# Optimization experiments

Measured on AMD Instinct MI355X. Metric: run time of the kernel, lower is better.

## Reference

```python
import jax, jax.numpy as jnp
import numpy as np

B, S, D, H = 4, 2048, 1024, 16
DH = D // H
MAX_SEQ = 2048
OUT = 1024


def setup_inputs() -> dict:
    key = jax.random.key(0)
    ks = jax.random.split(key, 10)
    inp = {
        "x": jax.random.normal(ks[0], (B, S, D), dtype=jnp.float32),
        "src_key_padding_mask": jnp.ones((B, S), dtype=jnp.float32),  # 1 = valid token
        "pos_emb": jax.random.normal(ks[1], (1, MAX_SEQ, D), dtype=jnp.float32),
        "ln_gamma": jnp.ones((D,), dtype=jnp.float32),
        "ln_beta": jnp.zeros((D,), dtype=jnp.float32),
        "in_proj_weight": jax.random.normal(ks[2], (3 * D, D), dtype=jnp.float32) * (1.0 / np.sqrt(D)),
        "in_proj_bias": jnp.zeros((3 * D,), dtype=jnp.float32),
        "out_proj_weight": jax.random.normal(ks[3], (D, D), dtype=jnp.float32) * (1.0 / np.sqrt(D)),
        "out_proj_bias": jnp.zeros((D,), dtype=jnp.float32),
        "to_out_weight": jax.random.normal(ks[4], (OUT, D), dtype=jnp.float32) * (1.0 / np.sqrt(D)),
        "to_out_bias": jnp.zeros((OUT,), dtype=jnp.float32),
    }
    return inp


def _layernorm(x, gamma, beta, eps=1e-5):
    mu = jnp.mean(x, axis=-1, keepdims=True)
    var = jnp.mean(jnp.square(x - mu), axis=-1, keepdims=True)
    return (x - mu) * jax.lax.rsqrt(var + eps) * gamma + beta


def reference(x, src_key_padding_mask, pos_emb, ln_gamma, ln_beta,
              in_proj_weight, in_proj_bias, out_proj_weight, out_proj_bias,
              to_out_weight, to_out_bias):
    seq = x.shape[1]
    xn = _layernorm(x, ln_gamma, ln_beta)
    xp = xn + pos_emb[:, :seq, :]  # [B,S,D]

    # PyTorch quirk: 1.0 - mask.long() is a FLOAT tensor -> treated as ADDITIVE mask.
    add_mask = (1.0 - src_key_padding_mask)[:, None, None, :]  # [B,1,1,S]

    qkv = xp @ in_proj_weight.T + in_proj_bias  # [B,S,3D]
    q, k, v = jnp.split(qkv, 3, axis=-1)
    # [B,H,S,DH]
    q = q.reshape(B, seq, H, DH).transpose(0, 2, 1, 3)
    k = k.reshape(B, seq, H, DH).transpose(0, 2, 1, 3)
    v = v.reshape(B, seq, H, DH).transpose(0, 2, 1, 3)

    scores = jnp.einsum("bhqd,bhkd->bhqk", q, k) / jnp.sqrt(jnp.float32(DH))
    scores = scores + add_mask
    attn = jax.nn.softmax(scores, axis=-1)
    o = jnp.einsum("bhqk,bhkd->bhqd", attn, v)  # [B,H,S,DH]
    o = o.transpose(0, 2, 1, 3).reshape(B, seq, D)
    attn_out = o @ out_proj_weight.T + out_proj_bias

    return (xp + attn_out) @ to_out_weight.T + to_out_bias
```

## Files before the change

### kernel.cpp

```cpp
#include <hip/hip_runtime.h>
#include <stdint.h>
#include <stddef.h>

typedef unsigned short u16;
typedef __bf16 bf16x8 __attribute__((ext_vector_type(8)));
typedef float floatx4 __attribute__((ext_vector_type(4)));

#define B_  4
#define S_  2048
#define D_  1024
#define H_  16
#define DH_ 64

__device__ __forceinline__ float b2f(u16 u) {
  union { unsigned u; float f; } c; c.u = ((unsigned)u) << 16; return c.f;
}
__device__ __forceinline__ u16 f2b(float f) {
  union { float f; unsigned u; } c; c.f = f;
  unsigned u = c.u;
  u += 0x7fffu + ((u >> 16) & 1u);
  return (u16)(u >> 16);
}

__device__ __forceinline__ void gld_lds16(const u16* g, u16* l) {
  __builtin_amdgcn_global_load_lds(
      (const __attribute__((address_space(1))) unsigned int*)g,
      (__attribute__((address_space(3))) unsigned int*)l, 16, 0, 0);
}

__global__ __launch_bounds__(256) void cvt_f32_bf16(
    const float* __restrict__ src, u16* __restrict__ dst, int n)
{
  int i = (blockIdx.x * 256 + threadIdx.x) * 4;
  if (i >= n) return;
  float4 v = *(const float4*)(src + i);
  u16 o[4] __attribute__((aligned(8)));
  o[0] = f2b(v.x); o[1] = f2b(v.y); o[2] = f2b(v.z); o[3] = f2b(v.w);
  *(uint2*)(dst + i) = *(uint2*)o;
}

__global__ __launch_bounds__(256) void ln_pos_kernel(
    const float* __restrict__ x, const float* __restrict__ pos,
    const float* __restrict__ gamma, const float* __restrict__ beta,
    u16* __restrict__ xp)
{
  const int row = blockIdx.x;
  const int s = row & (S_ - 1);
  const int t = threadIdx.x;
  const int lane = t & 63, w = t >> 6;

  float4 xv = *(const float4*)(x + (size_t)row * D_ + t * 4);
  float f[4] = {xv.x, xv.y, xv.z, xv.w};
  float sum = f[0] + f[1] + f[2] + f[3];
  float sq  = f[0]*f[0] + f[1]*f[1] + f[2]*f[2] + f[3]*f[3];
#pragma unroll
  for (int m = 1; m < 64; m <<= 1) {
    sum += __shfl_xor(sum, m);
    sq  += __shfl_xor(sq, m);
  }
  __shared__ float red[8];
  if (lane == 0) { red[w] = sum; red[4 + w] = sq; }
  __syncthreads();
  sum = red[0] + red[1] + red[2] + red[3];
  sq  = red[4] + red[5] + red[6] + red[7];
  const float mu = sum * (1.f / D_);
  const float rstd = rsqrtf(fmaxf(sq * (1.f / D_) - mu * mu, 0.f) + 1e-5f);

  float4 gv = *(const float4*)(gamma + t * 4);
  float4 bv = *(const float4*)(beta + t * 4);
  float4 pv = *(const float4*)(pos + (size_t)s * D_ + t * 4);
  float g[4] = {gv.x, gv.y, gv.z, gv.w};
  float bb[4] = {bv.x, bv.y, bv.z, bv.w};
  float pp[4] = {pv.x, pv.y, pv.z, pv.w};
  u16 ov[4] __attribute__((aligned(8)));
#pragma unroll
  for (int i = 0; i < 4; ++i)
    ov[i] = f2b((f[i] - mu) * rstd * g[i] + bb[i] + pp[i]);
  *(uint2*)(xp + (size_t)row * D_ + t * 4) = *(uint2*)ov;
}

template<int HAS_BIAS, int HAS_RES, int OUT_F32>
__global__ __launch_bounds__(256) void gemm_bt(
    const u16* A, const u16* __restrict__ Bm,
    const float* __restrict__ bias, const u16* res,
    void* Cv, int M, int N, int K, int lda, int ldc)
{
  __shared__ u16 As[128 * 32];
  __shared__ u16 Bs[128 * 32];
  const int tid = threadIdx.x;
  const int lane = tid & 63, w = tid >> 6;
  const int quad = lane >> 4, l4 = lane & 15;
  const int wm = (w >> 1) * 64, wn = (w & 1) * 64;
  const int m0 = blockIdx.y * 128, n0 = blockIdx.x * 128;

  const u16* Ag = A + (size_t)m0 * lda;
  const u16* Bg = Bm + (size_t)n0 * K;

  const int s0 = tid, s1 = tid + 256;
  const int r0 = s0 >> 2, c0 = ((s0 & 3) - (r0 >> 1)) & 3;
  const int r1 = s1 >> 2, c1 = ((s1 & 3) - (r1 >> 1)) & 3;
  const int pA = (quad + (l4 >> 1)) & 3;

  floatx4 acc[4][4] = {};

  for (int k0 = 0; k0 < K; k0 += 32) {
    __syncthreads();
    gld_lds16(Ag + (size_t)r0 * lda + k0 + c0 * 8, &As[s0 * 8]);
    gld_lds16(Ag + (size_t)r1 * lda + k0 + c1 * 8, &As[s1 * 8]);
    gld_lds16(Bg + (size_t)r0 * K + k0 + c0 * 8, &Bs[s0 * 8]);
    gld_lds16(Bg + (size_t)r1 * K + k0 + c1 * 8, &Bs[s1 * 8]);
    __syncthreads();
    bf16x8 af[4], bfr[4];
#pragma unroll
    for (int i = 0; i < 4; ++i)
      af[i] = *(const bf16x8*)&As[(wm + i * 16 + l4) * 32 + pA * 8];
#pragma unroll
    for (int j = 0; j < 4; ++j)
      bfr[j] = *(const bf16x8*)&Bs[(wn + j * 16 + l4) * 32 + pA * 8];
#pragma unroll
    for (int i = 0; i < 4; ++i)
#pragma unroll
      for (int j = 0; j < 4; ++j)
        acc[i][j] = __builtin_amdgcn_mfma_f32_16x16x32_bf16(af[i], bfr[j], acc[i][j], 0, 0, 0);
  }

#pragma unroll
  for (int i = 0; i < 4; ++i) {
#pragma unroll
    for (int j = 0; j < 4; ++j) {
      const int col = n0 + wn + j * 16 + l4;
      float bvv = 0.f;
      if (HAS_BIAS) bvv = bias[col];
#pragma unroll
      for (int r = 0; r < 4; ++r) {
        const int row = m0 + wm + i * 16 + quad * 4 + r;
        float v = acc[i][j][r] + bvv;
        if (HAS_RES) v += b2f(res[(size_t)row * ldc + col]);
        v = fminf(fmaxf(v, -60000.f), 60000.f);
        if (OUT_F32) ((float*)Cv)[(size_t)row * ldc + col] = v;
        else         ((u16*)Cv)[(size_t)row * ldc + col] = f2b(v);
      }
    }
  }
}

__global__ __launch_bounds__(256) void attn_kernel(
    u16* qkv, const float* __restrict__ mask)
{
  __shared__ u16 Qs[64 * 64];
  __shared__ u16 Ks[128 * 64];
  __shared__ u16 Vt[64 * 136];
  __shared__ u16 Ps[64 * 136];

  const int tid = threadIdx.x;
  const int lane = tid & 63, w = tid >> 6;
  const int quad = lane >> 4, l4 = lane & 15;
  const int qb = blockIdx.x;
  const int bh = blockIdx.y;
  const int b = bh >> 4, h = bh & 15;
  const int q0 = qb * 64;

  const size_t rstr = 3 * D_;
  u16* qbase = qkv + (size_t)b * S_ * rstr + h * DH_;

  {
    int sA = tid, sB = tid + 256;
    int ra = sA >> 3, ca = ((sA & 7) - ra) & 7;
    int rb = sB >> 3, cb = ((sB & 7) - rb) & 7;
    gld_lds16(qbase + (size_t)(q0 + ra) * rstr + ca * 8, &Qs[sA * 8]);
    gld_lds16(qbase + (size_t)(q0 + rb) * rstr + cb * 8, &Qs[sB * 8]);
  }

  floatx4 acc_o[4] = {};
  float l_run[4] = {0.f, 0.f, 0.f, 0.f};

  for (int j = 0; j < 16; ++j) {
    __syncthreads();
    const u16* kbase = qkv + ((size_t)b * S_ + j * 128) * rstr + D_ + h * DH_;
#pragma unroll
    for (int t = 0; t < 4; ++t) {
      int sidx = tid + t * 256;
      int r = sidx >> 3, ch = ((sidx & 7) - r) & 7;
      gld_lds16(kbase + (size_t)r * rstr + ch * 8, &Ks[sidx * 8]);
    }
    {
      const u16* vbase = qkv + ((size_t)b * S_ + j * 128) * rstr + 2 * D_ + h * DH_;
      int s = tid & 127, d0 = (tid >> 7) * 32;
      const u16* vp = vbase + (size_t)s * rstr + d0;
      u16 v[32] __attribute__((aligned(16)));
      *(uint4*)(v)      = *(const uint4*)(vp);
      *(uint4*)(v + 8)  = *(const uint4*)(vp + 8);
      *(uint4*)(v + 16) = *(const uint4*)(vp + 16);
      *(uint4*)(v + 24) = *(const uint4*)(vp + 24);
#pragma unroll
      for (int d = 0; d < 32; ++d) Vt[(d0 + d) * 136 + s] = v[d];
    }
    __syncthreads();

    floatx4 accs[8] = {};
#pragma unroll
    for (int kc = 0; kc < 2; ++kc) {
      const int rq = w * 16 + l4;
      bf16x8 af = *(const bf16x8*)&Qs[rq * 64 + (((kc * 4 + quad) + rq) & 7) * 8];
#pragma unroll
      for (int tj = 0; tj < 8; ++tj) {
        const int rk = tj * 16 + l4;
        bf16x8 bfr = *(const bf16x8*)&Ks[rk * 64 + (((kc * 4 + quad) + rk) & 7) * 8];
        accs[tj] = __builtin_amdgcn_mfma_f32_16x16x32_bf16(af, bfr, accs[tj], 0, 0, 0);
      }
    }

    const float* mrow = mask + (size_t)b * S_ + j * 128;
    float rsum[4] = {0.f, 0.f, 0.f, 0.f};
#pragma unroll
    for (int tj = 0; tj < 8; ++tj) {
      const float addm = 1.0f - mrow[tj * 16 + l4];
#pragma unroll
      for (int r = 0; r < 4; ++r) {
        float sc = fminf(accs[tj][r] * 0.125f + addm, 30.f);
        float p = __expf(sc);
        rsum[r] += p;
        Ps[(w * 16 + quad * 4 + r) * 136 + tj * 16 + l4] = f2b(p);
      }
    }
#pragma unroll
    for (int r = 0; r < 4; ++r) {
      float v = rsum[r];
      v += __shfl_xor(v, 1);
      v += __shfl_xor(v, 2);
      v += __shfl_xor(v, 4);
      v += __shfl_xor(v, 8);
      l_run[r] += v;
    }

    asm volatile("s_waitcnt lgkmcnt(0)" ::: "memory");

#pragma unroll
    for (int kc = 0; kc < 4; ++kc) {
      bf16x8 af = *(const bf16x8*)&Ps[(w * 16 + l4) * 136 + kc * 32 + quad * 8];
#pragma unroll
      for (int tn = 0; tn < 4; ++tn) {
        bf16x8 bfr = *(const bf16x8*)&Vt[(tn * 16 + l4) * 136 + kc * 32 + quad * 8];
        acc_o[tn] = __builtin_amdgcn_mfma_f32_16x16x32_bf16(af, bfr, acc_o[tn], 0, 0, 0);
      }
    }
  }

#pragma unroll
  for (int tn = 0; tn < 4; ++tn) {
#pragma unroll
    for (int r = 0; r < 4; ++r) {
      const int row = q0 + w * 16 + quad * 4 + r;
      const int col = h * DH_ + tn * 16 + l4;
      qkv[((size_t)b * S_ + row) * rstr + col] = f2b(acc_o[tn][r] / l_run[r]);
    }
  }
}

extern "C" void kernel_launch(void* const* d_in, const int* in_sizes, int n_in,
                              void* d_out, int out_size, void* d_ws, size_t ws_size,
                              hipStream_t stream) {
  const float* x    = (const float*)d_in[0];
  const float* mask = (const float*)d_in[1];
  const float* pos  = (const float*)d_in[2];
  const float* gam  = (const float*)d_in[3];
  const float* bet  = (const float*)d_in[4];
  const float* wqkv = (const float*)d_in[5];
  const float* bqkv = (const float*)d_in[6];
  const float* wo   = (const float*)d_in[7];
  const float* bo   = (const float*)d_in[8];
  const float* wt   = (const float*)d_in[9];
  const float* bt   = (const float*)d_in[10];
  float* out = (float*)d_out;

  char* ws = (char*)d_ws;
  u16* qkvb = (u16*)(ws);
  u16* xp   = (u16*)(ws + (size_t)50331648);

  u16* wqkv_b = (u16*)d_out;
  u16* wo_b   = (u16*)((char*)d_out + (size_t)6291456);
  u16* wt_b   = qkvb;

  const int nqkv = 3 * D_ * D_;
  const int nd   = D_ * D_;

  cvt_f32_bf16<<<nqkv / 1024, 256, 0, stream>>>(wqkv, wqkv_b, nqkv);
  cvt_f32_bf16<<<nd   / 1024, 256, 0, stream>>>(wo,   wo_b,   nd);
  ln_pos_kernel<<<B_ * S_, 256, 0, stream>>>(x, pos, gam, bet, xp);
  gemm_bt<1, 0, 0><<<dim3(3 * D_ / 128, B_ * S_ / 128), 256, 0, stream>>>(
      xp, wqkv_b, bqkv, nullptr, qkvb, B_ * S_, 3 * D_, D_, D_, 3 * D_);
  attn_kernel<<<dim3(S_ / 64, B_ * H_), 256, 0, stream>>>(qkvb, mask);
  gemm_bt<1, 1, 0><<<dim3(D_ / 128, B_ * S_ / 128), 256, 0, stream>>>(
      qkvb, wo_b, bo, xp, xp, B_ * S_, D_, D_, 3 * D_, D_);
  cvt_f32_bf16<<<nd / 1024, 256, 0, stream>>>(wt, wt_b, nd);
  gemm_bt<1, 0, 1><<<dim3(D_ / 128, B_ * S_ / 128), 256, 0, stream>>>(
      xp, wt_b, bt, nullptr, out, B_ * S_, D_, D_, D_, D_);
}
```

Measured before the change: 478.2 us.

## Keep Q and P fragments in registers in attention, drop Qs/Ps shared buffers

The attention kernel computes S^T (K as the A operand, Q held in registers), so each lane owns a query column. It turns probabilities into bf16 pairs with v_cvt_pk_bf16_f32 and rearranges them through permlane swaps into the A-operand layout of the PV MFMA, removing the Ps round trip through LDS and the Qs staging buffer. This cuts LDS traffic and footprint, allowing 4 blocks per CU via launch bounds, and adds setprio around the MFMAs. The cost is more register pressure and a reliance on exact lane-permutation semantics.

```diff
diff --git a/kernel.cpp b/kernel.cpp
--- a/kernel.cpp
+++ b/kernel.cpp
@@ -27,6 +27,17 @@
       (const __attribute__((address_space(1))) unsigned int*)g,
       (__attribute__((address_space(3))) unsigned int*)l, 16, 0, 0);
 }
+
+__device__ __forceinline__ unsigned cvtpk(float lo, float hi) {
+  unsigned r;
+  asm("v_cvt_pk_bf16_f32 %0, %1, %2" : "=v"(r) : "v"(lo), "v"(hi));
+  return r;
+}
+
+#define PL32(a, b) asm("v_permlane32_swap_b32 %0, %1" : "+v"(a), "+v"(b))
+#define PL16(a, b) asm("v_permlane16_swap_b32 %0, %1" : "+v"(a), "+v"(b))
+
+union B8 { unsigned u[4]; bf16x8 v; };
 
 __global__ __launch_bounds__(256) void cvt_f32_bf16(
     const float* __restrict__ src, u16* __restrict__ dst, int n)
@@ -144,13 +155,11 @@
   }
 }
 
-__global__ __launch_bounds__(256) void attn_kernel(
+__global__ __launch_bounds__(256, 4) void attn_kernel(
     u16* qkv, const float* __restrict__ mask)
 {
-  __shared__ u16 Qs[64 * 64];
   __shared__ u16 Ks[128 * 64];
   __shared__ u16 Vt[64 * 136];
-  __shared__ u16 Ps[64 * 136];
 
   const int tid = threadIdx.x;
   const int lane = tid & 63, w = tid >> 6;
@@ -163,16 +172,15 @@
   const size_t rstr = 3 * D_;
   u16* qbase = qkv + (size_t)b * S_ * rstr + h * DH_;
 
+  bf16x8 qfrag[2];
   {
-    int sA = tid, sB = tid + 256;
-    int ra = sA >> 3, ca = ((sA & 7) - ra) & 7;
-    int rb = sB >> 3, cb = ((sB & 7) - rb) & 7;
-    gld_lds16(qbase + (size_t)(q0 + ra) * rstr + ca * 8, &Qs[sA * 8]);
-    gld_lds16(qbase + (size_t)(q0 + rb) * rstr + cb * 8, &Qs[sB * 8]);
+    const u16* qp = qbase + (size_t)(q0 + w * 16 + l4) * rstr + quad * 8;
+    qfrag[0] = *(const bf16x8*)(qp);
+    qfrag[1] = *(const bf16x8*)(qp + 32);
   }
 
   floatx4 acc_o[4] = {};
-  float l_run[4] = {0.f, 0.f, 0.f, 0.f};
+  float l_run = 0.f;
 
   for (int j = 0; j < 16; ++j) {
     __syncthreads();
@@ -180,8 +188,8 @@
 #pragma unroll
     for (int t = 0; t < 4; ++t) {
       int sidx = tid + t * 256;
-      int r = sidx >> 3, ch = ((sidx & 7) - r) & 7;
-      gld_lds16(kbase + (size_t)r * rstr + ch * 8, &Ks[sidx * 8]);
+      int rr = sidx >> 3, ch = ((sidx & 7) - rr) & 7;
+      gld_lds16(kbase + (size_t)rr * rstr + ch * 8, &Ks[sidx * 8]);
     }
     {
       const u16* vbase = qkv + ((size_t)b * S_ + j * 128) * rstr + 2 * D_ + h * DH_;
@@ -199,60 +207,59 @@
 
     floatx4 accs[8] = {};
 #pragma unroll
-    for (int kc = 0; kc < 2; ++kc) {
-      const int rq = w * 16 + l4;
-      bf16x8 af = *(const bf16x8*)&Qs[rq * 64 + (((kc * 4 + quad) + rq) & 7) * 8];
+    for (int kc = 0; kc < 2; ++kc)
 #pragma unroll
       for (int tj = 0; tj < 8; ++tj) {
         const int rk = tj * 16 + l4;
-        bf16x8 bfr = *(const bf16x8*)&Ks[rk * 64 + (((kc * 4 + quad) + rk) & 7) * 8];
-        accs[tj] = __builtin_amdgcn_mfma_f32_16x16x32_bf16(af, bfr, accs[tj], 0, 0, 0);
+        bf16x8 kf = *(const bf16x8*)&Ks[rk * 64 + (((kc * 4 + quad) + rk) & 7) * 8];
+        accs[tj] = __builtin_amdgcn_mfma_f32_16x16x32_bf16(kf, qfrag[kc], accs[tj], 0, 0, 0);
       }
-    }
-
-    const float* mrow = mask + (size_t)b * S_ + j * 128;
-    float rsum[4] = {0.f, 0.f, 0.f, 0.f};
+
+    const float* mrow = mask + (size_t)b * S_ + j * 128 + quad * 4;
+    float rsum = 0.f;
+    unsigned pk[8][2];
 #pragma unroll
     for (int tj = 0; tj < 8; ++tj) {
-      const float addm = 1.0f - mrow[tj * 16 + l4];
-#pragma unroll
-      for (int r = 0; r < 4; ++r) {
-        float sc = fminf(accs[tj][r] * 0.125f + addm, 30.f);
-        float p = __expf(sc);
-        rsum[r] += p;
-        Ps[(w * 16 + quad * 4 + r) * 136 + tj * 16 + l4] = f2b(p);
-      }
-    }
-#pragma unroll
-    for (int r = 0; r < 4; ++r) {
-      float v = rsum[r];
-      v += __shfl_xor(v, 1);
-      v += __shfl_xor(v, 2);
-      v += __shfl_xor(v, 4);
-      v += __shfl_xor(v, 8);
-      l_run[r] += v;
-    }
-
-    asm volatile("s_waitcnt lgkmcnt(0)" ::: "memory");
+      float4 mv = *(const float4*)(mrow + tj * 16);
+      float p0 = __expf(fminf(fmaf(accs[tj][0], 0.125f, 1.0f - mv.x), 30.f));
+      float p1 = __expf(fminf(fmaf(accs[tj][1], 0.125f, 1.0f - mv.y), 30.f));
+      float p2 = __expf(fminf(fmaf(accs[tj][2], 0.125f, 1.0f - mv.z), 30.f));
+      float p3 = __expf(fminf(fmaf(accs[tj][3], 0.125f, 1.0f - mv.w), 30.f));
+      rsum += (p0 + p1) + (p2 + p3);
+      pk[tj][0] = cvtpk(p0, p1);
+      pk[tj][1] = cvtpk(p2, p3);
+    }
+    rsum += __shfl_xor(rsum, 16);
+    rsum += __shfl_xor(rsum, 32);
+    l_run += rsum;
 
 #pragma unroll
     for (int kc = 0; kc < 4; ++kc) {
-      bf16x8 af = *(const bf16x8*)&Ps[(w * 16 + l4) * 136 + kc * 32 + quad * 8];
+      unsigned x0 = pk[2 * kc][0], x1 = pk[2 * kc + 1][0];
+      unsigned y0 = pk[2 * kc][1], y1 = pk[2 * kc + 1][1];
+      PL32(x0, x1); PL32(y0, y1);
+      PL16(x0, x1); PL16(y0, y1);
+      B8 pa; pa.u[0] = x0; pa.u[1] = y0; pa.u[2] = x1; pa.u[3] = y1;
+      __builtin_amdgcn_s_setprio(1);
 #pragma unroll
       for (int tn = 0; tn < 4; ++tn) {
         bf16x8 bfr = *(const bf16x8*)&Vt[(tn * 16 + l4) * 136 + kc * 32 + quad * 8];
-        acc_o[tn] = __builtin_amdgcn_mfma_f32_16x16x32_bf16(af, bfr, acc_o[tn], 0, 0, 0);
+        acc_o[tn] = __builtin_amdgcn_mfma_f32_16x16x32_bf16(pa.v, bfr, acc_o[tn], 0, 0, 0);
       }
-    }
-  }
-
+      __builtin_amdgcn_s_setprio(0);
+    }
+  }
+
+  float inv[4];
+#pragma unroll
+  for (int r = 0; r < 4; ++r) inv[r] = 1.0f / __shfl(l_run, quad * 4 + r);
 #pragma unroll
   for (int tn = 0; tn < 4; ++tn) {
 #pragma unroll
     for (int r = 0; r < 4; ++r) {
       const int row = q0 + w * 16 + quad * 4 + r;
       const int col = h * DH_ + tn * 16 + l4;
-      qkv[((size_t)b * S_ + row) * rstr + col] = f2b(acc_o[tn][r] / l_run[r]);
+      qkv[((size_t)b * S_ + row) * rstr + col] = f2b(acc_o[tn][r] * inv[r]);
     }
   }
 }
```

Measured after the change: 415.5 us. -13.1%, faster.
